# Performance work log

Hardware: AMD Instinct MI355X
Metric: run time of the kernel (lower is better)

## Reference

```python
import jax, jax.numpy as jnp
import numpy as np

N = 40000          # nodes per type (dev, repo)
H, D = 8, 64       # heads, head dim
HID = H * D        # 512 hidden channels
OUT = 256
N_CONVS = 4        # 2 towers (res, link) x 2 layers
EDGE_TYPES = [(0, 1), (1, 0), (0, 0)]  # (src_type, dst_type)
SQRT_D = float(np.sqrt(D))


def _lin(x, w, b):
    return x @ w + b


def _seg_softmax(a, idx, n):
    m = jax.ops.segment_max(a, idx, num_segments=n)
    e = jnp.exp(a - m[idx])
    s = jax.ops.segment_sum(e, idx, num_segments=n)
    return e / (s[idx] + 1e-16)


def _hgt_conv(xs, edges, kw, kb, qw, qb, vw, vb, aw, ab, skip, a_rel, m_rel, p_rel):
    # xs: [x_dev, x_repo] each [N, HID]; edges: list of [2, E]
    k = [_lin(xs[t], kw[t], kb[t]).reshape(-1, H, D) for t in range(2)]
    q = [_lin(xs[t], qw[t], qb[t]).reshape(-1, H, D) for t in range(2)]
    v = [_lin(xs[t], vw[t], vb[t]).reshape(-1, H, D) for t in range(2)]
    out = [jnp.zeros_like(k[0]), jnp.zeros_like(k[1])]
    for r, (st, dt) in enumerate(EDGE_TYPES):
        src, dst = edges[r][0], edges[r][1]
        k_rel = jnp.einsum('nhd,hde->nhe', k[st], a_rel[r])
        v_rel = jnp.einsum('nhd,hde->nhe', v[st], m_rel[r])
        alpha = (q[dt][dst] * k_rel[src]).sum(-1) * p_rel[r] / SQRT_D  # [E, H]
        alpha = _seg_softmax(alpha, dst, N)
        msg = v_rel[src] * alpha[..., None]                            # [E, H, D]
        out[dt] = out[dt] + jax.ops.segment_sum(msg, dst, num_segments=N)
    res = []
    for t in range(2):
        o = _lin(jax.nn.gelu(out[t].reshape(-1, HID), approximate=False), aw[t], ab[t])
        g = jax.nn.sigmoid(skip[t])
        res.append(g * o + (1.0 - g) * xs[t])
    return res


def setup_inputs() -> dict:
    key = jax.random.key(0)
    ks = iter(jax.random.split(key, 48))
    def nrm(shape, scale=1.0):
        return jax.random.normal(next(ks), shape, dtype=jnp.float32) * scale
    E1, E2, E3, EP = 250000, 250000, 150000, 100000
    inp = {}
    inp['x_dev'] = nrm((N, HID))
    inp['x_repo'] = nrm((N, HID))
    inp['ei_dr'] = jax.random.randint(next(ks), (2, E1), 0, N, dtype=jnp.int32)
    inp['ei_rd'] = jax.random.randint(next(ks), (2, E2), 0, N, dtype=jnp.int32)
    inp['ei_dd'] = jax.random.randint(next(ks), (2, E3), 0, N, dtype=jnp.int32)
    inp['pos_edge'] = jax.random.randint(next(ks), (2, EP), 0, N, dtype=jnp.int32)
    inp['neg_edge'] = jax.random.randint(next(ks), (2, EP), 0, N, dtype=jnp.int32)
    s = 1.0 / np.sqrt(HID)
    for nm in ('k', 'q', 'v', 'a'):
        inp[nm + '_w'] = nrm((N_CONVS, 2, HID, HID), s)
        inp[nm + '_b'] = jnp.zeros((N_CONVS, 2, HID), jnp.float32)
    inp['skip'] = jnp.ones((N_CONVS, 2), jnp.float32)
    sd = 1.0 / np.sqrt(D)
    inp['a_rel'] = nrm((N_CONVS, 3, H, D, D), sd)
    inp['m_rel'] = nrm((N_CONVS, 3, H, D, D), sd)
    inp['p_rel'] = jnp.ones((N_CONVS, 3, H), jnp.float32)
    inp['reg_w1'] = nrm((HID, OUT), s); inp['reg_b1'] = jnp.zeros((OUT,), jnp.float32)
    inp['reg_w2'] = nrm((OUT, 1), 1.0 / np.sqrt(OUT)); inp['reg_b2'] = jnp.zeros((1,), jnp.float32)
    inp['src_w'] = nrm((HID, OUT), s); inp['src_b'] = jnp.zeros((OUT,), jnp.float32)
    inp['dst_w'] = nrm((HID, OUT), s); inp['dst_b'] = jnp.zeros((OUT,), jnp.float32)
    inp['fin_w'] = nrm((OUT, 1), 1.0 / np.sqrt(OUT)); inp['fin_b'] = jnp.zeros((1,), jnp.float32)
    return inp


def reference(x_dev, x_repo, ei_dr, ei_rd, ei_dd, pos_edge, neg_edge,
              k_w, k_b, q_w, q_b, v_w, v_b, a_w, a_b, skip,
              a_rel, m_rel, p_rel,
              reg_w1, reg_b1, reg_w2, reg_b2,
              src_w, src_b, dst_w, dst_b, fin_w, fin_b):
    edges = [ei_dr, ei_rd, ei_dd]

    def embed(conv_ids):
        xs = [x_dev, x_repo]
        for c in conv_ids:
            xs = _hgt_conv(xs, edges, k_w[c], k_b[c], q_w[c], q_b[c], v_w[c], v_b[c],
                           a_w[c], a_b[c], skip[c], a_rel[c], m_rel[c], p_rel[c])
            xs = [jax.nn.leaky_relu(x, 0.01) for x in xs]
        return xs

    res = embed([0, 1])   # embedding_res tower
    lnk = embed([2, 3])   # embedding_link tower
    emb_dev = res[0] + lnk[0]
    emb_repo = res[1] + lnk[1]

    fit_dev = _lin(_lin(emb_dev, reg_w1, reg_b1), reg_w2, reg_b2).squeeze(-1)
    fit_repo = _lin(_lin(emb_repo, reg_w1, reg_b1), reg_w2, reg_b2).squeeze(-1)

    def link(zs, zd):
        h = _lin(zs, src_w, src_b) * _lin(zd, dst_w, dst_b)
        return jax.nn.sigmoid(_lin(h, fin_w, fin_b)).squeeze(-1)

    pos = link(emb_dev[pos_edge[0]], emb_repo[pos_edge[1]])
    neg = link(emb_dev[neg_edge[0]], emb_repo[neg_edge[1]])
    score = jnp.concatenate([pos, neg], axis=0)
    return (fit_dev, fit_repo, score)
```

## Files before the change

### kernel.cpp

```cpp
#include <hip/hip_runtime.h>
#include <math.h>

#define NNODES 40000
#define NB ((size_t)20480000)
#define RPS 40004

typedef __attribute__((ext_vector_type(8))) short bf16x8;
typedef __attribute__((ext_vector_type(4))) float f32x4;

__device__ __forceinline__ ushort f2bf(float f) {
  unsigned u = __float_as_uint(f);
  u += 0x7FFFu + ((u >> 16) & 1u);
  return (ushort)(u >> 16);
}
__device__ __forceinline__ float b2f(ushort h) {
  return __uint_as_float((unsigned)h << 16);
}
__device__ __forceinline__ float gelu_f(float x) {
  return 0.5f * x * (1.0f + erff(x * 0.70710678118654752440f));
}

__device__ __forceinline__ void gll16(const ushort* g, ushort* l) {
  __builtin_amdgcn_global_load_lds(
      (const __attribute__((address_space(1))) unsigned int*)(const void*)g,
      (__attribute__((address_space(3))) unsigned int*)(void*)l, 16, 0, 0);
}

template<int EPI>
__global__ __launch_bounds__(256)
void gemm_bf16_kernel(const ushort* __restrict__ Av, const ushort* __restrict__ Bt,
                      const float* __restrict__ bias,
                      ushort* __restrict__ C0, ushort* __restrict__ C1,
                      int M, int PW,
                      const ushort* __restrict__ xprev, const float* __restrict__ skipv,
                      int nwgx)
{
  const int K = 512;
  __shared__ char smem[32768];
  ushort* Sm = (ushort*)smem;
  float*  Es = (float*)smem;

  const int nwg = (int)gridDim.x;
  const int q8 = nwg >> 3, r8 = nwg & 7;
  const int xcd = (int)blockIdx.x & 7, i8 = (int)blockIdx.x >> 3;
  const int logical = (xcd < r8 ? xcd * (q8 + 1) : r8 * (q8 + 1) + (xcd - r8) * q8) + i8;
  const int bm = (logical / nwgx) * 128;
  const int bnl = (logical % nwgx) * 128;
  const int pan = (bnl >= PW) ? 1 : 0;
  const int bn = bnl - pan * PW;
  ushort* __restrict__ C = pan ? C1 : C0;

  const int tid = threadIdx.x, lane = tid & 63, wave = tid >> 6;
  const int wr = (wave >> 1) * 64, wc = (wave & 1) * 64;
  const int fr = lane & 15, fq = lane >> 4;
  f32x4 acc[4][4] = {};

  const int rdsw = (fq ^ ((fr >> 1) & 3)) * 8;
  const int csrc = ((lane & 3) ^ ((lane >> 3) & 3)) * 8;
  const int r0 = wave * 32 + (lane >> 2);
  int ra0 = bm + r0;      if (ra0 >= M) ra0 = M - 1;
  int ra1 = bm + r0 + 16; if (ra1 >= M) ra1 = M - 1;
  const ushort* ga0 = Av + (size_t)ra0 * K + csrc;
  const ushort* ga1 = Av + (size_t)ra1 * K + csrc;
  const ushort* gb0 = Bt + (size_t)(bnl + r0) * K + csrc;
  const ushort* gb1 = Bt + (size_t)(bnl + r0 + 16) * K + csrc;
  ushort* la0[2] = {Sm + wave * 1024,        Sm + 8192 + wave * 1024};
  ushort* la1[2] = {la0[0] + 512,            la0[1] + 512};
  ushort* lb0[2] = {Sm + 4096 + wave * 1024, Sm + 12288 + wave * 1024};
  ushort* lb1[2] = {lb0[0] + 512,            lb0[1] + 512};

  gll16(ga0, la0[0]); gll16(ga1, la1[0]); gll16(gb0, lb0[0]); gll16(gb1, lb1[0]);
  ga0 += 32; ga1 += 32; gb0 += 32; gb1 += 32;
  gll16(ga0, la0[1]); gll16(ga1, la1[1]); gll16(gb0, lb0[1]); gll16(gb1, lb1[1]);
  ga0 += 32; ga1 += 32; gb0 += 32; gb1 += 32;

  #pragma unroll
  for (int it = 0; it < 16; ++it) {
    const int cur = it & 1;
    if (it < 15) asm volatile("s_waitcnt vmcnt(4)" ::: "memory");
    else         asm volatile("s_waitcnt vmcnt(0)" ::: "memory");
    __builtin_amdgcn_s_barrier();
    const ushort* Ab = Sm + cur * 8192;
    const ushort* Bb = Ab + 4096;
    bf16x8 af[4], bfv[4];
    #pragma unroll
    for (int i = 0; i < 4; ++i) {
      af[i]  = *(const bf16x8*)&Ab[(wr + i * 16 + fr) * 32 + rdsw];
      bfv[i] = *(const bf16x8*)&Bb[(wc + i * 16 + fr) * 32 + rdsw];
    }
    asm volatile("s_waitcnt lgkmcnt(0)" ::: "memory");
    __builtin_amdgcn_s_barrier();
    if (it < 14) {
      gll16(ga0, la0[cur]); gll16(ga1, la1[cur]); gll16(gb0, lb0[cur]); gll16(gb1, lb1[cur]);
      ga0 += 32; ga1 += 32; gb0 += 32; gb1 += 32;
    }
    #pragma unroll
    for (int mi = 0; mi < 4; ++mi)
      #pragma unroll
      for (int ni = 0; ni < 4; ++ni)
        acc[mi][ni] = __builtin_amdgcn_mfma_f32_16x16x32_bf16(af[mi], bfv[ni], acc[mi][ni], 0, 0, 0);
  }
  __syncthreads();

  float gate = 0.f, og = 0.f;
  if (EPI == 2) { gate = 1.f / (1.f + __expf(-skipv[0])); og = 1.f - gate; }
  #pragma unroll
  for (int qr = 0; qr < 4; ++qr) {
    __syncthreads();
    #pragma unroll
    for (int mi = 0; mi < 4; ++mi) {
      if (((wr + mi * 16) >> 5) != qr) continue;
      const int lr = ((wr + mi * 16) & 31) + fq * 4;
      #pragma unroll
      for (int ni = 0; ni < 4; ++ni) {
        const int col = wc + ni * 16 + fr;
        #pragma unroll
        for (int r = 0; r < 4; ++r)
          Es[(lr + r) * 132 + col] = acc[mi][ni][r];
      }
    }
    __syncthreads();
    const int lrow = tid >> 3;
    const int c0 = (tid & 7) * 16;
    const int grow = bm + qr * 32 + lrow;
    if (grow < M) {
      float v[16];
      #pragma unroll
      for (int j = 0; j < 4; ++j)
        *(float4*)&v[j * 4] = *(const float4*)&Es[lrow * 132 + c0 + j * 4];
      if (EPI == 1 || EPI == 2) {
        #pragma unroll
        for (int j = 0; j < 4; ++j) {
          float4 b4 = *(const float4*)(bias + bnl + c0 + j * 4);
          v[j*4] += b4.x; v[j*4+1] += b4.y; v[j*4+2] += b4.z; v[j*4+3] += b4.w;
        }
      }
      size_t base = (size_t)grow * PW + bn + c0;
      if (EPI == 2) {
        uint4 x0 = *(const uint4*)(xprev + base);
        uint4 x1 = *(const uint4*)(xprev + base + 8);
        #pragma unroll
        for (int j = 0; j < 8; ++j) {
          unsigned w = (j < 4) ? ((const unsigned*)&x0)[j] : ((const unsigned*)&x1)[j - 4];
          float a  = gate * v[2*j]   + og * __uint_as_float(w << 16);
          float bq = gate * v[2*j+1] + og * __uint_as_float(w & 0xFFFF0000u);
          v[2*j]   = a  > 0.f ? a  : 0.01f * a;
          v[2*j+1] = bq > 0.f ? bq : 0.01f * bq;
        }
      }
      if (EPI == 4) {
        uint4 x0 = *(const uint4*)(C + base);
        uint4 x1 = *(const uint4*)(C + base + 8);
        #pragma unroll
        for (int j = 0; j < 8; ++j) {
          unsigned w = (j < 4) ? ((const unsigned*)&x0)[j] : ((const unsigned*)&x1)[j - 4];
          v[2*j]   += __uint_as_float(w << 16);
          v[2*j+1] += __uint_as_float(w & 0xFFFF0000u);
        }
      }
      ushort ob[16];
      #pragma unroll
      for (int j = 0; j < 16; ++j) ob[j] = f2bf(v[j]);
      *(uint4*)(C + base)     = *(uint4*)&ob[0];
      *(uint4*)(C + base + 8) = *(uint4*)&ob[8];
    }
  }
}

__global__ __launch_bounds__(256)
void transpose_w_batch(const float* __restrict__ q_w, const float* __restrict__ a_w,
                       const float* __restrict__ src_w, const float* __restrict__ dst_w,
                       ushort* __restrict__ wqT, ushort* __restrict__ waT,
                       ushort* __restrict__ srcwT, ushort* __restrict__ dstwT)
{
  const int z = blockIdx.z;
  const float* W; ushort* Wt; int N;
  if (z < 8)       { W = q_w + (size_t)z * 262144;       Wt = wqT + (size_t)z * 262144;       N = 512; }
  else if (z < 16) { W = a_w + (size_t)(z - 8) * 262144; Wt = waT + (size_t)(z - 8) * 262144; N = 512; }
  else if (z == 16){ W = src_w; Wt = srcwT; N = 256; }
  else             { W = dst_w; Wt = dstwT; N = 256; }
  int bn = blockIdx.x * 32, bk = blockIdx.y * 32;
  if (bn >= N) return;
  __shared__ float t[32][33];
  int x = threadIdx.x & 31, y = threadIdx.x >> 5;
  #pragma unroll
  for (int yy = y; yy < 32; yy += 8) t[yy][x] = W[(size_t)(bk + yy) * N + bn + x];
  __syncthreads();
  #pragma unroll
  for (int yy = y; yy < 32; yy += 8) Wt[(size_t)(bn + yy) * 512 + bk + x] = f2bf(t[x][yy]);
}

__global__ __launch_bounds__(256)
void fold_rel_batch(const float* __restrict__ k_w, const float* __restrict__ k_b,
                    const float* __restrict__ v_w, const float* __restrict__ v_b,
                    const float* __restrict__ a_rel, const float* __restrict__ m_rel,
                    ushort* __restrict__ wkvT, float* __restrict__ bfuse)
{
  const int z = blockIdx.z;
  const int kv = z / 12, i = z % 12;
  const int c = i / 3, r = i % 3;
  const int st_tab[3] = {0, 1, 0};
  const int stp = st_tab[r];
  const float* Win  = (kv ? v_w : k_w) + (size_t)(c * 2 + stp) * 262144;
  const float* bin  = (kv ? v_b : k_b) + (size_t)(c * 2 + stp) * 512;
  const float* Arel = (kv ? m_rel : a_rel) + (size_t)i * 32768;
  ushort* W2t = wkvT + (size_t)i * 524288 + (size_t)kv * 262144;
  float*  b2  = bfuse + i * 1024 + kv * 512;
  const int h = blockIdx.x, kc = blockIdx.y;

  __shared__ float Wl[64][65];
  __shared__ float Al[4096];
  for (int j = threadIdx.x; j < 4096; j += 256) Al[j] = Arel[(size_t)h * 4096 + j];
  {
    const int kk = threadIdx.x >> 2, d0 = (threadIdx.x & 3) * 16;
    const float* src = Win + (size_t)(kc * 64 + kk) * 512 + h * 64 + d0;
    #pragma unroll
    for (int j = 0; j < 4; ++j)
      *(float4*)&Wl[kk][d0 + j * 4] = *(const float4*)(src + j * 4);
  }
  __syncthreads();
  const int wave = threadIdx.x >> 6, lane = threadIdx.x & 63;
  #pragma unroll 4
  for (int rr = 0; rr < 16; ++rr) {
    const int e = wave * 16 + rr;
    float acc = 0.f;
    #pragma unroll
    for (int d = 0; d < 64; ++d) acc = fmaf(Wl[lane][d], Al[d * 64 + e], acc);
    W2t[(size_t)(h * 64 + e) * 512 + kc * 64 + lane] = f2bf(acc);
  }
  if (kc == 0 && wave == 0) {
    float acc = 0.f;
    #pragma unroll
    for (int d = 0; d < 64; ++d) acc = fmaf(bin[h * 64 + d], Al[d * 64 + lane], acc);
    b2[h * 64 + lane] = acc;
  }
}

__global__ __launch_bounds__(256)
void make_wfit_kernel(const float* __restrict__ w1, const float* __restrict__ b1,
                      const float* __restrict__ w2, const float* __restrict__ b2,
                      float* __restrict__ wfit)
{
  for (int k = threadIdx.x; k < 512; k += 256) {
    float acc = 0.f;
    for (int j = 0; j < 256; ++j) acc = fmaf(w1[(size_t)k * 256 + j], w2[j], acc);
    wfit[k] = acc;
  }
  if (threadIdx.x == 0) {
    float acc = 0.f;
    for (int j = 0; j < 256; ++j) acc = fmaf(b1[j], w2[j], acc);
    wfit[512] = acc + b2[0];
  }
}

__global__ __launch_bounds__(256)
void hist_batch(const int* __restrict__ d0, const int* __restrict__ d1,
                const int* __restrict__ d2, unsigned* __restrict__ cnt3)
{
  const int z = blockIdx.z;
  const int* dst = (z == 0) ? d0 : (z == 1) ? d1 : d2;
  const int E = (z == 2) ? 150000 : 250000;
  unsigned* cnt = cnt3 + (size_t)z * NNODES;
  for (int i = blockIdx.x * 256 + threadIdx.x; i < E; i += gridDim.x * 256)
    atomicAdd(&cnt[dst[i]], 1u);
}

__global__ __launch_bounds__(256)
void scan_batch(const unsigned* __restrict__ cnt3, unsigned* __restrict__ rowptr3,
                unsigned* __restrict__ woff3)
{
  const int z = blockIdx.x;
  const unsigned* cnt = cnt3 + (size_t)z * NNODES;
  unsigned* rowptr = rowptr3 + (size_t)z * RPS;
  unsigned* woff   = woff3 + (size_t)z * NNODES;
  __shared__ unsigned csum[256];
  const int t = threadIdx.x;
  const int lo = t * 160, hi = (lo + 160 < NNODES) ? lo + 160 : NNODES;
  unsigned s = 0;
  for (int i = lo; i < hi; i += 4) {
    uint4 v = *(const uint4*)&cnt[i];
    s += v.x + v.y + v.z + v.w;
  }
  csum[t] = s;
  __syncthreads();
  if (t == 0) {
    unsigned run = 0;
    for (int j = 0; j < 256; ++j) { unsigned v = csum[j]; csum[j] = run; run += v; }
    rowptr[NNODES] = run;
  }
  __syncthreads();
  unsigned run = csum[t];
  for (int i = lo; i < hi; i += 4) {
    uint4 cv = *(const uint4*)&cnt[i];
    uint4 rp;
    rp.x = run; run += cv.x;
    rp.y = run; run += cv.y;
    rp.z = run; run += cv.z;
    rp.w = run; run += cv.w;
    *(uint4*)&rowptr[i] = rp;
    *(uint4*)&woff[i]   = rp;
  }
}

__global__ __launch_bounds__(256)
void fill_batch(const int* __restrict__ d0, const int* __restrict__ d1,
                const int* __restrict__ d2, unsigned* __restrict__ woff3,
                unsigned* __restrict__ order)
{
  const int z = blockIdx.z;
  const int* dst = (z == 0) ? d0 : (z == 1) ? d1 : d2;
  const int E = (z == 2) ? 150000 : 250000;
  unsigned* woff = woff3 + (size_t)z * NNODES;
  unsigned* ord  = order + ((z == 0) ? 0 : (z == 1) ? 250000 : 500000);
  for (int i = blockIdx.x * 256 + threadIdx.x; i < E; i += gridDim.x * 256) {
    unsigned slot = atomicAdd(&woff[dst[i]], 1u);
    ord[slot] = (unsigned)i;
  }
}

__global__ __launch_bounds__(256)
void edge_softmax_kernel(const ushort* __restrict__ q, const ushort* __restrict__ kr,
                         const int* __restrict__ srcp,
                         const unsigned* __restrict__ rowptr, const unsigned* __restrict__ order,
                         const float* __restrict__ prel, float* __restrict__ alpha,
                         float* __restrict__ ssumA)
{
  int d = (int)((blockIdx.x * 256u + threadIdx.x) >> 6);
  int lane = threadIdx.x & 63;
  if (d >= NNODES) return;
  unsigned start = rowptr[d], end = rowptr[d + 1];
  if (start == end) return;
  const int h = lane >> 3;
  const float pscale = prel[h] * 0.125f;

  uint4 qv = *(const uint4*)(q + (size_t)d * 512 + lane * 8);
  const unsigned* pq = (const unsigned*)&qv;
  float qf[8];
  #pragma unroll
  for (int j = 0; j < 4; ++j) {
    qf[2*j]   = __uint_as_float(pq[j] << 16);
    qf[2*j+1] = __uint_as_float(pq[j] & 0xFFFF0000u);
  }

  float m = -3e38f;
  for (unsigned idx = start; idx < end; ++idx) {
    int e = (int)order[idx];
    int s = srcp[e];
    uint4 kv = *(const uint4*)(kr + (size_t)s * 512 + lane * 8);
    const unsigned* pk = (const unsigned*)&kv;
    float acc = 0.f;
    #pragma unroll
    for (int j = 0; j < 4; ++j) {
      acc = fmaf(qf[2*j],   __uint_as_float(pk[j] << 16),         acc);
      acc = fmaf(qf[2*j+1], __uint_as_float(pk[j] & 0xFFFF0000u), acc);
    }
    acc += __shfl_xor(acc, 1);
    acc += __shfl_xor(acc, 2);
    acc += __shfl_xor(acc, 4);
    float a = acc * pscale;
    if ((lane & 7) == 0) alpha[(size_t)idx * 8 + h] = a;
    m = fmaxf(m, a);
  }
  asm volatile("s_waitcnt vmcnt(0)" ::: "memory");
  if ((lane & 7) == 0) {
    float ssum = 0.f;
    for (unsigned idx = start; idx < end; ++idx) {
      float ev = __expf(alpha[(size_t)idx * 8 + h] - m);
      alpha[(size_t)idx * 8 + h] = ev;
      ssum += ev;
    }
    ssumA[(size_t)d * 8 + h] = 1.f / (ssum + 1e-16f);
  }
}

template<int ACCUM, int GELU>
__global__ __launch_bounds__(256)
void gather_msg_kernel(const float* __restrict__ alpha, const float* __restrict__ ssumA,
                       const ushort* __restrict__ vrel, const int* __restrict__ srcp,
                       const unsigned* __restrict__ rowptr, const unsigned* __restrict__ order,
                       const ushort* __restrict__ accin, ushort* __restrict__ outp)
{
  int d = (int)((blockIdx.x * 256u + threadIdx.x) >> 6);
  int lane = threadIdx.x & 63;
  if (d >= NNODES) return;
  unsigned start = rowptr[d], end = rowptr[d + 1];
  const int h = lane >> 3;
  const float rs = ssumA[(size_t)d * 8 + h];
  float acc[8] = {};
  for (unsigned idx = start; idx < end; ++idx) {
    int e = (int)order[idx];
    int s = srcp[e];
    float w = alpha[(size_t)idx * 8 + h] * rs;
    uint4 vv = *(const uint4*)(vrel + (size_t)s * 512 + lane * 8);
    const unsigned* pv = (const unsigned*)&vv;
    #pragma unroll
    for (int j = 0; j < 4; ++j) {
      acc[2*j]   = fmaf(__uint_as_float(pv[j] << 16),         w, acc[2*j]);
      acc[2*j+1] = fmaf(__uint_as_float(pv[j] & 0xFFFF0000u), w, acc[2*j+1]);
    }
  }
  if (ACCUM) {
    uint4 old = *(const uint4*)(accin + (size_t)d * 512 + lane * 8);
    const unsigned* po = (const unsigned*)&old;
    #pragma unroll
    for (int j = 0; j < 4; ++j) {
      acc[2*j]   += __uint_as_float(po[j] << 16);
      acc[2*j+1] += __uint_as_float(po[j] & 0xFFFF0000u);
    }
  }
  ushort t[8];
  #pragma unroll
  for (int j = 0; j < 8; ++j) t[j] = f2bf(GELU ? gelu_f(acc[j]) : acc[j]);
  *(uint4*)(outp + (size_t)d * 512 + lane * 8) = *(uint4*)t;
}

template<int MODE>
__global__ __launch_bounds__(256)
void fitdot_kernel(const ushort* __restrict__ cur, const float* __restrict__ wfit,
                   float* __restrict__ out, int M)
{
  int row = (int)((blockIdx.x * 256u + threadIdx.x) >> 6);
  int lane = threadIdx.x & 63;
  if (row >= M) return;
  uint4 v = *(const uint4*)(cur + (size_t)row * 512 + lane * 8);
  const unsigned* pv = (const unsigned*)&v;
  float wreg[8];
  *(float4*)wreg       = *(const float4*)(wfit + lane * 8);
  *(float4*)(wreg + 4) = *(const float4*)(wfit + lane * 8 + 4);
  float acc = 0.f;
  #pragma unroll
  for (int j = 0; j < 4; ++j) {
    acc = fmaf(__uint_as_float(pv[j] << 16),         wreg[2 * j],     acc);
    acc = fmaf(__uint_as_float(pv[j] & 0xFFFF0000u), wreg[2 * j + 1], acc);
  }
  #pragma unroll
  for (int off = 1; off < 64; off <<= 1) acc += __shfl_xor(acc, off);
  if (lane == 0) {
    if (MODE == 0) out[row] = acc;
    else           out[row] += acc + wfit[512];
  }
}

__global__ __launch_bounds__(256)
void link_score_kernel(const ushort* __restrict__ se, const ushort* __restrict__ de,
                       const float* __restrict__ sb, const float* __restrict__ db,
                       const int* __restrict__ si, const int* __restrict__ di,
                       int E, const float* __restrict__ fw, const float* __restrict__ fb,
                       float* __restrict__ out)
{
  int wv = (int)((blockIdx.x * 256u + threadIdx.x) >> 6);
  int lane = threadIdx.x & 63;
  if (wv >= E) return;
  int s = si[wv], d = di[wv];
  ushort4 a = *(const ushort4*)(se + (size_t)s * 256 + lane * 4);
  ushort4 b = *(const ushort4*)(de + (size_t)d * 256 + lane * 4);
  float4 s4 = *(const float4*)(sb + lane * 4);
  float4 d4 = *(const float4*)(db + lane * 4);
  float4 w4 = *(const float4*)(fw + lane * 4);
  float acc = (b2f(a.x) + s4.x) * (b2f(b.x) + d4.x) * w4.x
            + (b2f(a.y) + s4.y) * (b2f(b.y) + d4.y) * w4.y
            + (b2f(a.z) + s4.z) * (b2f(b.z) + d4.z) * w4.z
            + (b2f(a.w) + s4.w) * (b2f(b.w) + d4.w) * w4.w;
  #pragma unroll
  for (int off = 1; off < 64; off <<= 1) acc += __shfl_xor(acc, off);
  if (lane == 0) out[wv] = 1.f / (1.f + __expf(-(acc + fb[0])));
}

__global__ __launch_bounds__(256)
void f32_to_bf16_kernel(const float* __restrict__ in, ushort* __restrict__ out, int n4)
{
  for (int i = blockIdx.x * 256 + threadIdx.x; i < n4; i += gridDim.x * 256) {
    float4 v = ((const float4*)in)[i];
    ushort4 o; o.x = f2bf(v.x); o.y = f2bf(v.y); o.z = f2bf(v.z); o.w = f2bf(v.w);
    ((ushort4*)out)[i] = o;
  }
}

__global__ void diag_kernel(float* __restrict__ out, float v)
{
  if (threadIdx.x == 0 && blockIdx.x == 0) out[0] = v;
}

extern "C" void kernel_launch(void* const* d_in, const int* in_sizes, int n_in,
                              void* d_out, int out_size, void* d_ws, size_t ws_size,
                              hipStream_t stream)
{
  const float* x_dev  = (const float*)d_in[0];
  const float* x_repo = (const float*)d_in[1];
  const int* ei[3] = {(const int*)d_in[2], (const int*)d_in[3], (const int*)d_in[4]};
  const int  Ecnt[3] = {250000, 250000, 150000};
  const int* pos_e = (const int*)d_in[5];
  const int* neg_e = (const int*)d_in[6];
  const float* k_w = (const float*)d_in[7];  const float* k_b = (const float*)d_in[8];
  const float* q_w = (const float*)d_in[9];  const float* q_b = (const float*)d_in[10];
  const float* v_w = (const float*)d_in[11]; const float* v_b = (const float*)d_in[12];
  const float* a_w = (const float*)d_in[13]; const float* a_b = (const float*)d_in[14];
  const float* skip  = (const float*)d_in[15];
  const float* a_rel = (const float*)d_in[16];
  const float* m_rel = (const float*)d_in[17];
  const float* p_rel = (const float*)d_in[18];
  const float* reg_w1 = (const float*)d_in[19]; const float* reg_b1 = (const float*)d_in[20];
  const float* reg_w2 = (const float*)d_in[21]; const float* reg_b2 = (const float*)d_in[22];
  const float* src_w  = (const float*)d_in[23]; const float* src_b  = (const float*)d_in[24];
  const float* dst_w  = (const float*)d_in[25]; const float* dst_b  = (const float*)d_in[26];
  const float* fin_w  = (const float*)d_in[27]; const float* fin_b  = (const float*)d_in[28];
  float* out = (float*)d_out;

  const size_t SE = (size_t)NNODES * 256;
  const size_t tail_bytes =
      2000000ull * 4
    + (size_t)8 * 262144 * 2
    + (size_t)8 * 262144 * 2
    + (size_t)12 * 524288 * 2
    + 131072ull * 2 * 2
    + 12288ull * 4
    + 516ull * 4
    + (size_t)3 * RPS * 4
    + 650000ull * 4
    + (size_t)3 * NNODES * 4 * 2
    + 320000ull * 4;
  const size_t need_fused  = (6 * NB + 2 * SE) * 2 + tail_bytes;
  const size_t need_nofuse = (5 * NB + 2 * SE) * 2 + tail_bytes;
  int FUSED;
  if      (ws_size >= need_fused)  FUSED = 1;
  else if (ws_size >= need_nofuse) FUSED = 0;
  else {
    diag_kernel<<<1, 64, 0, stream>>>(out, 1000.0f + (float)(ws_size / 1000000));
    return;
  }

  ushort* st   = (ushort*)d_ws;
  ushort* cur0 = st;
  ushort* cur1 = st + NB;
  ushort* S1   = st + 2 * NB;
  ushort* S2   = st + 3 * NB;
  ushort* msgB = st + 4 * NB;
  ushort* S3   = FUSED ? (st + 5 * NB) : S2;
  ushort* se   = st + (FUSED ? 6 : 5) * NB;
  ushort* de   = se + SE;
  float*  alpha = (float*)(de + SE);
  ushort* wqT   = (ushort*)(alpha + 2000000);
  ushort* waT   = wqT + (size_t)8 * 262144;
  ushort* wkvT  = waT + (size_t)8 * 262144;
  ushort* srcwT = wkvT + (size_t)12 * 524288;
  ushort* dstwT = srcwT + 131072;
  float*  bfuse = (float*)(dstwT + 131072);
  float*  wfit  = bfuse + 12288;
  unsigned* rowptr3 = (unsigned*)(wfit + 516);
  unsigned* order   = rowptr3 + (size_t)3 * RPS;
  unsigned* cnt3    = order + 650000;
  unsigned* woff3   = cnt3 + (size_t)3 * NNODES;
  float*    ssumA   = (float*)(woff3 + (size_t)3 * NNODES);
  const size_t ord_off[3] = {0, 250000, 500000};

  transpose_w_batch<<<dim3(16, 16, 18), 256, 0, stream>>>(q_w, a_w, src_w, dst_w,
                                                          wqT, waT, srcwT, dstwT);
  fold_rel_batch<<<dim3(8, 8, 24), 256, 0, stream>>>(k_w, k_b, v_w, v_b, a_rel, m_rel,
                                                     wkvT, bfuse);
  make_wfit_kernel<<<1, 256, 0, stream>>>(reg_w1, reg_b1, reg_w2, reg_b2, wfit);
  hipMemsetAsync(cnt3, 0, (size_t)3 * NNODES * 4, stream);
  hist_batch<<<dim3(977, 1, 3), 256, 0, stream>>>(ei[0] + Ecnt[0], ei[1] + Ecnt[1],
                                                  ei[2] + Ecnt[2], cnt3);
  scan_batch<<<3, 256, 0, stream>>>(cnt3, rowptr3, woff3);
  fill_batch<<<dim3(977, 1, 3), 256, 0, stream>>>(ei[0] + Ecnt[0], ei[1] + Ecnt[1],
                                                  ei[2] + Ecnt[2], woff3, order);

  auto gemmQ = [&](const ushort* A, int t, ushort* C) {
    gemm_bf16_kernel<1><<<1252, 256, 0, stream>>>(A, wqT + (size_t)t * 262144,
        q_b + (size_t)t * 512, C, C, NNODES, 512, nullptr, nullptr, 4);
  };
  auto gemmKV = [&](int i, const ushort* A) {
    gemm_bf16_kernel<1><<<2504, 256, 0, stream>>>(A, wkvT + (size_t)i * 524288,
        bfuse + (size_t)i * 1024, S2, S3, NNODES, 512, nullptr, nullptr, 8);
  };
  auto gemmK = [&](int i, const ushort* A) {
    gemm_bf16_kernel<1><<<1252, 256, 0, stream>>>(A, wkvT + (size_t)i * 524288,
        bfuse + (size_t)i * 1024, S2, S2, NNODES, 512, nullptr, nullptr, 4);
  };
  auto gemmV = [&](int i, const ushort* A) {
    gemm_bf16_kernel<1><<<1252, 256, 0, stream>>>(A, wkvT + (size_t)i * 524288 + 262144,
        bfuse + (size_t)i * 1024 + 512, S2, S2, NNODES, 512, nullptr, nullptr, 4);
  };
  auto gemmA = [&](int t, ushort* curb) {
    gemm_bf16_kernel<2><<<1252, 256, 0, stream>>>(S1, waT + (size_t)t * 262144,
        a_b + (size_t)t * 512, curb, curb, NNODES, 512, curb, skip + t, 4);
  };

  auto esm = [&](int c, int r, const ushort* qp) {
    edge_softmax_kernel<<<10000, 256, 0, stream>>>(
        qp, S2, ei[r], rowptr3 + (size_t)r * RPS, order + ord_off[r],
        p_rel + (size_t)(c * 3 + r) * 8, alpha, ssumA);
  };
  auto gath = [&](int r, int accum, int gelu, const ushort* vrel, ushort* outp) {
    const unsigned* rp = rowptr3 + (size_t)r * RPS;
    const unsigned* od = order + ord_off[r];
    if (accum) {
      if (gelu) gather_msg_kernel<1, 1><<<10000, 256, 0, stream>>>(alpha, ssumA, vrel, ei[r], rp, od, msgB, outp);
      else      gather_msg_kernel<1, 0><<<10000, 256, 0, stream>>>(alpha, ssumA, vrel, ei[r], rp, od, msgB, outp);
    } else {
      if (gelu) gather_msg_kernel<0, 1><<<10000, 256, 0, stream>>>(alpha, ssumA, vrel, ei[r], rp, od, nullptr, outp);
      else      gather_msg_kernel<0, 0><<<10000, 256, 0, stream>>>(alpha, ssumA, vrel, ei[r], rp, od, nullptr, outp);
    }
  };

  auto run_conv = [&](int c) {
    const int t0 = c * 2, t1 = c * 2 + 1;
    gemmQ(cur0, t0, S1);
    if (FUSED) { gemmKV(c * 3 + 1, cur1); esm(c, 1, S1); }
    else       { gemmK(c * 3 + 1, cur1); esm(c, 1, S1); gemmV(c * 3 + 1, cur1); }
    gath(1, 0, 0, S3, msgB);
    if (FUSED) { gemmKV(c * 3 + 2, cur0); esm(c, 2, S1); }
    else       { gemmK(c * 3 + 2, cur0); esm(c, 2, S1); gemmV(c * 3 + 2, cur0); }
    gath(2, 1, 1, S3, S1);
    if (FUSED) { gemmKV(c * 3 + 0, cur0); gemmQ(cur1, t1, msgB); esm(c, 0, msgB); }
    else       { gemmK(c * 3 + 0, cur0); gemmQ(cur1, t1, msgB); esm(c, 0, msgB);
                 gemmV(c * 3 + 0, cur0); }
    gemmA(t0, cur0);
    gath(0, 0, 1, S3, S1);
    gemmA(t1, cur1);
  };

  f32_to_bf16_kernel<<<2048, 256, 0, stream>>>(x_dev,  cur0, (int)(NB / 4));
  f32_to_bf16_kernel<<<2048, 256, 0, stream>>>(x_repo, cur1, (int)(NB / 4));
  run_conv(0);
  run_conv(1);
  fitdot_kernel<0><<<10000, 256, 0, stream>>>(cur0, wfit, out, NNODES);
  fitdot_kernel<0><<<10000, 256, 0, stream>>>(cur1, wfit, out + NNODES, NNODES);
  gemm_bf16_kernel<3><<<626, 256, 0, stream>>>(cur0, srcwT, nullptr, se, se, NNODES, 256, nullptr, nullptr, 2);
  gemm_bf16_kernel<3><<<626, 256, 0, stream>>>(cur1, dstwT, nullptr, de, de, NNODES, 256, nullptr, nullptr, 2);

  f32_to_bf16_kernel<<<2048, 256, 0, stream>>>(x_dev,  cur0, (int)(NB / 4));
  f32_to_bf16_kernel<<<2048, 256, 0, stream>>>(x_repo, cur1, (int)(NB / 4));
  run_conv(2);
  run_conv(3);
  fitdot_kernel<1><<<10000, 256, 0, stream>>>(cur0, wfit, out, NNODES);
  fitdot_kernel<1><<<10000, 256, 0, stream>>>(cur1, wfit, out + NNODES, NNODES);
  gemm_bf16_kernel<4><<<626, 256, 0, stream>>>(cur0, srcwT, nullptr, se, se, NNODES, 256, nullptr, nullptr, 2);
  gemm_bf16_kernel<4><<<626, 256, 0, stream>>>(cur1, dstwT, nullptr, de, de, NNODES, 256, nullptr, nullptr, 2);

  link_score_kernel<<<25000, 256, 0, stream>>>(se, de, src_b, dst_b, pos_e, pos_e + 100000,
                                               100000, fin_w, fin_b, out + 80000);
  link_score_kernel<<<25000, 256, 0, stream>>>(se, de, src_b, dst_b, neg_e, neg_e + 100000,
                                               100000, fin_w, fin_b, out + 180000);
}
```

Before: 3.222 ms.

## Fuse edge softmax and message gather with online softmax over half-head K/V slices

Replaces the separate edge-softmax and gather kernels with one kernel that computes scores, runs an online (running-max) softmax and accumulates V in a single pass over each destination's incoming edges. This removes the alpha and ssum buffers and one extra pass over the neighbour list. To make it work, the folded K/V weights are laid out so that each GEMM produces K and V for four heads interleaved in one 512-wide row, and each relation is processed in two half-head passes. That keeps the K and V gathers on the same row but doubles the edge-kernel launches and issues smaller 8-byte loads per lane.

```diff
diff --git a/kernel.cpp b/kernel.cpp
--- a/kernel.cpp
+++ b/kernel.cpp
@@ -31,7 +31,7 @@
 void gemm_bf16_kernel(const ushort* __restrict__ Av, const ushort* __restrict__ Bt,
                       const float* __restrict__ bias,
                       ushort* __restrict__ C0, ushort* __restrict__ C1,
-                      int M, int PW,
+                      int M, int PW, int RS,
                       const ushort* __restrict__ xprev, const float* __restrict__ skipv,
                       int nwgx)
 {
@@ -135,7 +135,7 @@
           v[j*4] += b4.x; v[j*4+1] += b4.y; v[j*4+2] += b4.z; v[j*4+3] += b4.w;
         }
       }
-      size_t base = (size_t)grow * PW + bn + c0;
+      size_t base = (size_t)grow * RS + bn + c0;
       if (EPI == 2) {
         uint4 x0 = *(const uint4*)(xprev + base);
         uint4 x1 = *(const uint4*)(xprev + base + 8);
@@ -204,9 +204,10 @@
   const float* Win  = (kv ? v_w : k_w) + (size_t)(c * 2 + stp) * 262144;
   const float* bin  = (kv ? v_b : k_b) + (size_t)(c * 2 + stp) * 512;
   const float* Arel = (kv ? m_rel : a_rel) + (size_t)i * 32768;
-  ushort* W2t = wkvT + (size_t)i * 524288 + (size_t)kv * 262144;
-  float*  b2  = bfuse + i * 1024 + kv * 512;
   const int h = blockIdx.x, kc = blockIdx.y;
+  ushort* W2t = wkvT + (size_t)i * 524288 + (size_t)(h >> 2) * 262144
+              + (size_t)(kv * 256 + (h & 3) * 64) * 512;
+  float*  b2  = bfuse + i * 1024 + (h >> 2) * 512 + kv * 256 + (h & 3) * 64;
 
   __shared__ float Wl[64][65];
   __shared__ float Al[4096];
@@ -226,13 +227,13 @@
     float acc = 0.f;
     #pragma unroll
     for (int d = 0; d < 64; ++d) acc = fmaf(Wl[lane][d], Al[d * 64 + e], acc);
-    W2t[(size_t)(h * 64 + e) * 512 + kc * 64 + lane] = f2bf(acc);
+    W2t[(size_t)e * 512 + kc * 64 + lane] = f2bf(acc);
   }
   if (kc == 0 && wave == 0) {
     float acc = 0.f;
     #pragma unroll
     for (int d = 0; d < 64; ++d) acc = fmaf(bin[h * 64 + d], Al[d * 64 + lane], acc);
-    b2[h * 64 + lane] = acc;
+    b2[lane] = acc;
   }
 }
 
@@ -318,100 +319,67 @@
   }
 }
 
-__global__ __launch_bounds__(256)
-void edge_softmax_kernel(const ushort* __restrict__ q, const ushort* __restrict__ kr,
-                         const int* __restrict__ srcp,
-                         const unsigned* __restrict__ rowptr, const unsigned* __restrict__ order,
-                         const float* __restrict__ prel, float* __restrict__ alpha,
-                         float* __restrict__ ssumA)
+template<int ACCUM, int GELU>
+__global__ __launch_bounds__(256)
+void fused_edge_kernel(const ushort* __restrict__ q, const ushort* __restrict__ KVh,
+                       const int* __restrict__ srcp,
+                       const unsigned* __restrict__ rowptr, const unsigned* __restrict__ order,
+                       const float* __restrict__ prel, int hs,
+                       const ushort* __restrict__ accin, ushort* __restrict__ outp)
 {
   int d = (int)((blockIdx.x * 256u + threadIdx.x) >> 6);
   int lane = threadIdx.x & 63;
   if (d >= NNODES) return;
   unsigned start = rowptr[d], end = rowptr[d + 1];
-  if (start == end) return;
-  const int h = lane >> 3;
-  const float pscale = prel[h] * 0.125f;
-
-  uint4 qv = *(const uint4*)(q + (size_t)d * 512 + lane * 8);
-  const unsigned* pq = (const unsigned*)&qv;
-  float qf[8];
-  #pragma unroll
-  for (int j = 0; j < 4; ++j) {
-    qf[2*j]   = __uint_as_float(pq[j] << 16);
-    qf[2*j+1] = __uint_as_float(pq[j] & 0xFFFF0000u);
-  }
-
-  float m = -3e38f;
+  const int hl = lane >> 4;
+  const int off = hl * 64 + (lane & 15) * 4;
+  const float pscale = prel[hs * 4 + hl] * 0.125f;
+  const size_t obase = (size_t)d * 512 + hs * 256 + off;
+
+  uint2 qv = *(const uint2*)(q + obase);
+  float qf0 = __uint_as_float(qv.x << 16),         qf1 = __uint_as_float(qv.x & 0xFFFF0000u);
+  float qf2 = __uint_as_float(qv.y << 16),         qf3 = __uint_as_float(qv.y & 0xFFFF0000u);
+
+  float m = -3e38f, ssum = 0.f;
+  float a0 = 0.f, a1 = 0.f, a2 = 0.f, a3 = 0.f;
   for (unsigned idx = start; idx < end; ++idx) {
-    int e = (int)order[idx];
-    int s = srcp[e];
-    uint4 kv = *(const uint4*)(kr + (size_t)s * 512 + lane * 8);
-    const unsigned* pk = (const unsigned*)&kv;
-    float acc = 0.f;
-    #pragma unroll
-    for (int j = 0; j < 4; ++j) {
-      acc = fmaf(qf[2*j],   __uint_as_float(pk[j] << 16),         acc);
-      acc = fmaf(qf[2*j+1], __uint_as_float(pk[j] & 0xFFFF0000u), acc);
-    }
-    acc += __shfl_xor(acc, 1);
-    acc += __shfl_xor(acc, 2);
-    acc += __shfl_xor(acc, 4);
-    float a = acc * pscale;
-    if ((lane & 7) == 0) alpha[(size_t)idx * 8 + h] = a;
-    m = fmaxf(m, a);
-  }
-  asm volatile("s_waitcnt vmcnt(0)" ::: "memory");
-  if ((lane & 7) == 0) {
-    float ssum = 0.f;
-    for (unsigned idx = start; idx < end; ++idx) {
-      float ev = __expf(alpha[(size_t)idx * 8 + h] - m);
-      alpha[(size_t)idx * 8 + h] = ev;
-      ssum += ev;
-    }
-    ssumA[(size_t)d * 8 + h] = 1.f / (ssum + 1e-16f);
-  }
-}
-
-template<int ACCUM, int GELU>
-__global__ __launch_bounds__(256)
-void gather_msg_kernel(const float* __restrict__ alpha, const float* __restrict__ ssumA,
-                       const ushort* __restrict__ vrel, const int* __restrict__ srcp,
-                       const unsigned* __restrict__ rowptr, const unsigned* __restrict__ order,
-                       const ushort* __restrict__ accin, ushort* __restrict__ outp)
-{
-  int d = (int)((blockIdx.x * 256u + threadIdx.x) >> 6);
-  int lane = threadIdx.x & 63;
-  if (d >= NNODES) return;
-  unsigned start = rowptr[d], end = rowptr[d + 1];
-  const int h = lane >> 3;
-  const float rs = ssumA[(size_t)d * 8 + h];
-  float acc[8] = {};
-  for (unsigned idx = start; idx < end; ++idx) {
-    int e = (int)order[idx];
-    int s = srcp[e];
-    float w = alpha[(size_t)idx * 8 + h] * rs;
-    uint4 vv = *(const uint4*)(vrel + (size_t)s * 512 + lane * 8);
-    const unsigned* pv = (const unsigned*)&vv;
-    #pragma unroll
-    for (int j = 0; j < 4; ++j) {
-      acc[2*j]   = fmaf(__uint_as_float(pv[j] << 16),         w, acc[2*j]);
-      acc[2*j+1] = fmaf(__uint_as_float(pv[j] & 0xFFFF0000u), w, acc[2*j+1]);
-    }
-  }
+    int sn = srcp[(int)order[idx]];
+    const ushort* row = KVh + (size_t)sn * 512 + off;
+    uint2 kv = *(const uint2*)row;
+    uint2 vv = *(const uint2*)(row + 256);
+    float dot =      qf0 * __uint_as_float(kv.x << 16);
+    dot = fmaf(qf1, __uint_as_float(kv.x & 0xFFFF0000u), dot);
+    dot = fmaf(qf2, __uint_as_float(kv.y << 16),         dot);
+    dot = fmaf(qf3, __uint_as_float(kv.y & 0xFFFF0000u), dot);
+    dot += __shfl_xor(dot, 1);
+    dot += __shfl_xor(dot, 2);
+    dot += __shfl_xor(dot, 4);
+    dot += __shfl_xor(dot, 8);
+    float a = dot * pscale;
+    if (a > m) {
+      float r = __expf(m - a);
+      ssum *= r; a0 *= r; a1 *= r; a2 *= r; a3 *= r;
+      m = a;
+    }
+    float w = __expf(a - m);
+    ssum += w;
+    a0 = fmaf(w, __uint_as_float(vv.x << 16),         a0);
+    a1 = fmaf(w, __uint_as_float(vv.x & 0xFFFF0000u), a1);
+    a2 = fmaf(w, __uint_as_float(vv.y << 16),         a2);
+    a3 = fmaf(w, __uint_as_float(vv.y & 0xFFFF0000u), a3);
+  }
+  float rs = 1.f / (ssum + 1e-16f);
+  float o0 = a0 * rs, o1 = a1 * rs, o2 = a2 * rs, o3 = a3 * rs;
   if (ACCUM) {
-    uint4 old = *(const uint4*)(accin + (size_t)d * 512 + lane * 8);
-    const unsigned* po = (const unsigned*)&old;
-    #pragma unroll
-    for (int j = 0; j < 4; ++j) {
-      acc[2*j]   += __uint_as_float(po[j] << 16);
-      acc[2*j+1] += __uint_as_float(po[j] & 0xFFFF0000u);
-    }
-  }
-  ushort t[8];
-  #pragma unroll
-  for (int j = 0; j < 8; ++j) t[j] = f2bf(GELU ? gelu_f(acc[j]) : acc[j]);
-  *(uint4*)(outp + (size_t)d * 512 + lane * 8) = *(uint4*)t;
+    uint2 old = *(const uint2*)(accin + obase);
+    o0 += __uint_as_float(old.x << 16);  o1 += __uint_as_float(old.x & 0xFFFF0000u);
+    o2 += __uint_as_float(old.y << 16);  o3 += __uint_as_float(old.y & 0xFFFF0000u);
+  }
+  if (GELU) { o0 = gelu_f(o0); o1 = gelu_f(o1); o2 = gelu_f(o2); o3 = gelu_f(o3); }
+  uint2 ov;
+  ov.x = (unsigned)f2bf(o0) | ((unsigned)f2bf(o1) << 16);
+  ov.y = (unsigned)f2bf(o2) | ((unsigned)f2bf(o3) << 16);
+  *(uint2*)(outp + obase) = ov;
 }
 
 template<int MODE>
@@ -507,39 +475,15 @@
   float* out = (float*)d_out;
 
   const size_t SE = (size_t)NNODES * 256;
-  const size_t tail_bytes =
-      2000000ull * 4
-    + (size_t)8 * 262144 * 2
-    + (size_t)8 * 262144 * 2
-    + (size_t)12 * 524288 * 2
-    + 131072ull * 2 * 2
-    + 12288ull * 4
-    + 516ull * 4
-    + (size_t)3 * RPS * 4
-    + 650000ull * 4
-    + (size_t)3 * NNODES * 4 * 2
-    + 320000ull * 4;
-  const size_t need_fused  = (6 * NB + 2 * SE) * 2 + tail_bytes;
-  const size_t need_nofuse = (5 * NB + 2 * SE) * 2 + tail_bytes;
-  int FUSED;
-  if      (ws_size >= need_fused)  FUSED = 1;
-  else if (ws_size >= need_nofuse) FUSED = 0;
-  else {
-    diag_kernel<<<1, 64, 0, stream>>>(out, 1000.0f + (float)(ws_size / 1000000));
-    return;
-  }
-
   ushort* st   = (ushort*)d_ws;
   ushort* cur0 = st;
   ushort* cur1 = st + NB;
   ushort* S1   = st + 2 * NB;
   ushort* S2   = st + 3 * NB;
-  ushort* msgB = st + 4 * NB;
-  ushort* S3   = FUSED ? (st + 5 * NB) : S2;
-  ushort* se   = st + (FUSED ? 6 : 5) * NB;
+  ushort* KVh  = st + 4 * NB;
+  ushort* se   = st + 5 * NB;
   ushort* de   = se + SE;
-  float*  alpha = (float*)(de + SE);
-  ushort* wqT   = (ushort*)(alpha + 2000000);
+  ushort* wqT   = de + SE;
   ushort* waT   = wqT + (size_t)8 * 262144;
   ushort* wkvT  = waT + (size_t)8 * 262144;
   ushort* srcwT = wkvT + (size_t)12 * 524288;
@@ -550,7 +494,11 @@
   unsigned* order   = rowptr3 + (size_t)3 * RPS;
   unsigned* cnt3    = order + 650000;
   unsigned* woff3   = cnt3 + (size_t)3 * NNODES;
-  float*    ssumA   = (float*)(woff3 + (size_t)3 * NNODES);
+  const size_t need = (size_t)((char*)(woff3 + (size_t)3 * NNODES) - (char*)d_ws);
+  if (ws_size < need) {
+    diag_kernel<<<1, 64, 0, stream>>>(out, 1000.0f + (float)(ws_size / 1000000));
+    return;
+  }
   const size_t ord_off[3] = {0, 250000, 500000};
 
   transpose_w_batch<<<dim3(16, 16, 18), 256, 0, stream>>>(q_w, a_w, src_w, dst_w,
@@ -567,57 +515,41 @@
 
   auto gemmQ = [&](const ushort* A, int t, ushort* C) {
     gemm_bf16_kernel<1><<<1252, 256, 0, stream>>>(A, wqT + (size_t)t * 262144,
-        q_b + (size_t)t * 512, C, C, NNODES, 512, nullptr, nullptr, 4);
+        q_b + (size_t)t * 512, C, C, NNODES, 512, 512, nullptr, nullptr, 4);
   };
-  auto gemmKV = [&](int i, const ushort* A) {
-    gemm_bf16_kernel<1><<<2504, 256, 0, stream>>>(A, wkvT + (size_t)i * 524288,
-        bfuse + (size_t)i * 1024, S2, S3, NNODES, 512, nullptr, nullptr, 8);
+  auto gemmKVh = [&](int i, int hs, const ushort* A) {
+    gemm_bf16_kernel<1><<<1252, 256, 0, stream>>>(A,
+        wkvT + (size_t)i * 524288 + (size_t)hs * 262144,
+        bfuse + (size_t)i * 1024 + hs * 512,
+        KVh, KVh + 256, NNODES, 256, 512, nullptr, nullptr, 4);
   };
-  auto gemmK = [&](int i, const ushort* A) {
-    gemm_bf16_kernel<1><<<1252, 256, 0, stream>>>(A, wkvT + (size_t)i * 524288,
-        bfuse + (size_t)i * 1024, S2, S2, NNODES, 512, nullptr, nullptr, 4);
+  auto gemmA = [&](int t, const ushort* Abuf, ushort* curb) {
+    gemm_bf16_kernel<2><<<1252, 256, 0, stream>>>(Abuf, waT + (size_t)t * 262144,
+        a_b + (size_t)t * 512, curb, curb, NNODES, 512, 512, curb, skip + t, 4);
   };
-  auto gemmV = [&](int i, const ushort* A) {
-    gemm_bf16_kernel<1><<<1252, 256, 0, stream>>>(A, wkvT + (size_t)i * 524288 + 262144,
-        bfuse + (size_t)i * 1024 + 512, S2, S2, NNODES, 512, nullptr, nullptr, 4);
-  };
-  auto gemmA = [&](int t, ushort* curb) {
-    gemm_bf16_kernel<2><<<1252, 256, 0, stream>>>(S1, waT + (size_t)t * 262144,
-        a_b + (size_t)t * 512, curb, curb, NNODES, 512, curb, skip + t, 4);
-  };
-
-  auto esm = [&](int c, int r, const ushort* qp) {
-    edge_softmax_kernel<<<10000, 256, 0, stream>>>(
-        qp, S2, ei[r], rowptr3 + (size_t)r * RPS, order + ord_off[r],
-        p_rel + (size_t)(c * 3 + r) * 8, alpha, ssumA);
-  };
-  auto gath = [&](int r, int accum, int gelu, const ushort* vrel, ushort* outp) {
-    const unsigned* rp = rowptr3 + (size_t)r * RPS;
-    const unsigned* od = order + ord_off[r];
-    if (accum) {
-      if (gelu) gather_msg_kernel<1, 1><<<10000, 256, 0, stream>>>(alpha, ssumA, vrel, ei[r], rp, od, msgB, outp);
-      else      gather_msg_kernel<1, 0><<<10000, 256, 0, stream>>>(alpha, ssumA, vrel, ei[r], rp, od, msgB, outp);
-    } else {
-      if (gelu) gather_msg_kernel<0, 1><<<10000, 256, 0, stream>>>(alpha, ssumA, vrel, ei[r], rp, od, nullptr, outp);
-      else      gather_msg_kernel<0, 0><<<10000, 256, 0, stream>>>(alpha, ssumA, vrel, ei[r], rp, od, nullptr, outp);
-    }
-  };
 
   auto run_conv = [&](int c) {
-    const int t0 = c * 2, t1 = c * 2 + 1;
+    const int t0 = 2 * c, t1 = 2 * c + 1;
+    const int i0 = 3 * c, i1 = 3 * c + 1, i2 = 3 * c + 2;
     gemmQ(cur0, t0, S1);
-    if (FUSED) { gemmKV(c * 3 + 1, cur1); esm(c, 1, S1); }
-    else       { gemmK(c * 3 + 1, cur1); esm(c, 1, S1); gemmV(c * 3 + 1, cur1); }
-    gath(1, 0, 0, S3, msgB);
-    if (FUSED) { gemmKV(c * 3 + 2, cur0); esm(c, 2, S1); }
-    else       { gemmK(c * 3 + 2, cur0); esm(c, 2, S1); gemmV(c * 3 + 2, cur0); }
-    gath(2, 1, 1, S3, S1);
-    if (FUSED) { gemmKV(c * 3 + 0, cur0); gemmQ(cur1, t1, msgB); esm(c, 0, msgB); }
-    else       { gemmK(c * 3 + 0, cur0); gemmQ(cur1, t1, msgB); esm(c, 0, msgB);
-                 gemmV(c * 3 + 0, cur0); }
-    gemmA(t0, cur0);
-    gath(0, 0, 1, S3, S1);
-    gemmA(t1, cur1);
+    for (int hs = 0; hs < 2; ++hs) {
+      gemmKVh(i1, hs, cur1);
+      fused_edge_kernel<0, 0><<<10000, 256, 0, stream>>>(S1, KVh, ei[1],
+          rowptr3 + RPS, order + ord_off[1], p_rel + (size_t)i1 * 8, hs, nullptr, S2);
+    }
+    for (int hs = 0; hs < 2; ++hs) {
+      gemmKVh(i2, hs, cur0);
+      fused_edge_kernel<1, 1><<<10000, 256, 0, stream>>>(S1, KVh, ei[2],
+          rowptr3 + 2 * RPS, order + ord_off[2], p_rel + (size_t)i2 * 8, hs, S2, S2);
+    }
+    gemmQ(cur1, t1, S1);
+    for (int hs = 0; hs < 2; ++hs) {
+      gemmKVh(i0, hs, cur0);
+      fused_edge_kernel<0, 1><<<10000, 256, 0, stream>>>(S1, KVh, ei[0],
+          rowptr3, order + ord_off[0], p_rel + (size_t)i0 * 8, hs, nullptr, S1);
+    }
+    gemmA(t0, S2, cur0);
+    gemmA(t1, S1, cur1);
   };
 
   f32_to_bf16_kernel<<<2048, 256, 0, stream>>>(x_dev,  cur0, (int)(NB / 4));
@@ -626,8 +558,8 @@
   run_conv(1);
   fitdot_kernel<0><<<10000, 256, 0, stream>>>(cur0, wfit, out, NNODES);
   fitdot_kernel<0><<<10000, 256, 0, stream>>>(cur1, wfit, out + NNODES, NNODES);
-  gemm_bf16_kernel<3><<<626, 256, 0, stream>>>(cur0, srcwT, nullptr, se, se, NNODES, 256, nullptr, nullptr, 2);
-  gemm_bf16_kernel<3><<<626, 256, 0, stream>>>(cur1, dstwT, nullptr, de, de, NNODES, 256, nullptr, nullptr, 2);
+  gemm_bf16_kernel<3><<<626, 256, 0, stream>>>(cur0, srcwT, nullptr, se, se, NNODES, 256, 256, nullptr, nullptr, 2);
+  gemm_bf16_kernel<3><<<626, 256, 0, stream>>>(cur1, dstwT, nullptr, de, de, NNODES, 256, 256, nullptr, nullptr, 2);
 
   f32_to_bf16_kernel<<<2048, 256, 0, stream>>>(x_dev,  cur0, (int)(NB / 4));
   f32_to_bf16_kernel<<<2048, 256, 0, stream>>>(x_repo, cur1, (int)(NB / 4));
@@ -635,8 +567,8 @@
   run_conv(3);
   fitdot_kernel<1><<<10000, 256, 0, stream>>>(cur0, wfit, out, NNODES);
   fitdot_kernel<1><<<10000, 256, 0, stream>>>(cur1, wfit, out + NNODES, NNODES);
-  gemm_bf16_kernel<4><<<626, 256, 0, stream>>>(cur0, srcwT, nullptr, se, se, NNODES, 256, nullptr, nullptr, 2);
-  gemm_bf16_kernel<4><<<626, 256, 0, stream>>>(cur1, dstwT, nullptr, de, de, NNODES, 256, nullptr, nullptr, 2);
+  gemm_bf16_kernel<4><<<626, 256, 0, stream>>>(cur0, srcwT, nullptr, se, se, NNODES, 256, 256, nullptr, nullptr, 2);
+  gemm_bf16_kernel<4><<<626, 256, 0, stream>>>(cur1, dstwT, nullptr, de, de, NNODES, 256, 256, nullptr, nullptr, 2);
 
   link_score_kernel<<<25000, 256, 0, stream>>>(se, de, src_b, dst_b, pos_e, pos_e + 100000,
                                                100000, fin_w, fin_b, out + 80000);
```

Result: no change. 3.221 ms (-0.0%).
